# Performance work log

Hardware: AMD Instinct MI355X
Metric: run time of the kernel (lower is better)

## Reference

```python
import jax, jax.numpy as jnp
import numpy as np

D_IN, D, HEADS, DH, DEPTH, NMEM = 1024, 512, 4, 128, 2, 60


def _layernorm(x, g, b, eps=1e-5):
    m = x.mean(-1, keepdims=True)
    v = ((x - m) ** 2).mean(-1, keepdims=True)
    return (x - m) * jax.lax.rsqrt(v + eps) * g + b


def setup_inputs() -> dict:
    key = jax.random.key(0)
    ks = jax.random.split(key, 24)
    r = lambda i, shape, s=0.02: jax.random.normal(ks[i], shape, jnp.float32) * s
    inner = HEADS * DH  # 512
    inp = {
        "x": jax.random.normal(ks[0], (8, 2048, D_IN), jnp.float32),
        # Temporal conv1d (kernel=3, pad=1), WIO layout
        "conv_w": r(1, (3, D_IN, D)),
        "conv_b": jnp.zeros((D,), jnp.float32),
        # 2 transformer layers, stacked on leading axis
        "ln1_g": jnp.ones((DEPTH, D), jnp.float32),
        "ln1_b": jnp.zeros((DEPTH, D), jnp.float32),
        "qkv_w": r(2, (DEPTH, D, inner * 4)),
        "out_w": r(3, (DEPTH, 2 * inner, D)),
        "out_b": jnp.zeros((DEPTH, D), jnp.float32),
        "ln2_g": jnp.ones((DEPTH, D), jnp.float32),
        "ln2_b": jnp.zeros((DEPTH, D), jnp.float32),
        "ff_w1": r(4, (DEPTH, D, D)),
        "ff_b1": jnp.zeros((DEPTH, D), jnp.float32),
        "ff_w2": r(5, (DEPTH, D, D)),
        "ff_b2": jnp.zeros((DEPTH, D), jnp.float32),
        # memory banks (uniform +-1/sqrt(dim) per reset_parameters)
        "amem": jax.random.uniform(ks[6], (NMEM, D), jnp.float32, -1.0, 1.0) / np.sqrt(D),
        "nmem": jax.random.uniform(ks[7], (NMEM, D), jnp.float32, -1.0, 1.0) / np.sqrt(D),
        "enc_w": r(8, (D, D)),
        "enc_b": jnp.zeros((D,), jnp.float32),
        "cls_w1": r(9, (2 * D, 128)),
        "cls_b1": jnp.zeros((128,), jnp.float32),
        "cls_w2": r(10, (128, 1)),
        "cls_b2": jnp.zeros((1,), jnp.float32),
    }
    return inp


def _forward(x, conv_w, conv_b, ln1_g, ln1_b, qkv_w, out_w, out_b,
             ln2_g, ln2_b, ff_w1, ff_b1, ff_w2, ff_b2,
             amem, nmem, enc_w, enc_b, cls_w1, cls_b1, cls_w2, cls_b2):
    b, n, _ = x.shape
    # Temporal: conv1d k=3 same padding + ReLU -> (b, n, 512)
    h = jax.lax.conv_general_dilated(x, conv_w, (1,), "SAME",
                                     dimension_numbers=("NWC", "WIO", "NWC")) + conv_b
    h = jax.nn.relu(h)

    # fixed-decay attention matrix (same for all layers): exp(-|i-j|/e), col-sum normalized
    idx = jnp.arange(n, dtype=jnp.float32)
    A2 = jnp.exp(-jnp.abs(idx[:, None] - idx[None, :]) / jnp.e)  # (n, n)
    A2 = A2 / A2.sum(-1)  # torch broadcast: divide along last dim by row-sums (symmetric)

    scale = DH ** -0.5
    for l in range(DEPTH):
        xn = _layernorm(h, ln1_g[l], ln1_b[l])
        qkvt = xn @ qkv_w[l]  # (b, n, 4*inner)
        q, k, v, t = jnp.split(qkvt, 4, axis=-1)
        reshape = lambda a: a.reshape(b, n, HEADS, DH).transpose(0, 2, 1, 3)  # bhnd
        q, k, v, t = map(reshape, (q, k, v, t))
        attn1 = jax.nn.softmax(jnp.einsum("bhnd,bhmd->bhnm", q, k) * scale, axis=-1)
        o1 = jnp.einsum("bhnm,bhmd->bhnd", attn1, v)
        o2 = jnp.einsum("nm,bhmd->bhnd", A2, t)
        o = jnp.concatenate([o1, o2], axis=-1)  # (b, h, n, 2*dh)
        o = o.transpose(0, 2, 1, 3).reshape(b, n, 2 * HEADS * DH)
        h = o @ out_w[l] + out_b[l] + h
        xn2 = _layernorm(h, ln2_g[l], ln2_b[l])
        ff = jax.nn.gelu(xn2 @ ff_w1[l] + ff_b1[l], approximate=False) @ ff_w2[l] + ff_b2[l]
        h = ff + h

    # memory retrieval (augment path only; temporal_att discarded in Test forward)
    mscale = 1.0 / np.sqrt(D)
    a_att = jax.nn.sigmoid(jnp.einsum("btd,kd->btk", h, amem) * mscale)
    n_att = jax.nn.sigmoid(jnp.einsum("btd,kd->btk", h, nmem) * mscale)
    a_aug = jnp.einsum("btk,kd->btd", a_att, amem) @ enc_w + enc_b
    n_aug = jnp.einsum("btk,kd->btd", n_att, nmem) @ enc_w + enc_b

    z = jnp.concatenate([h, a_aug + n_aug], axis=-1)  # (b, n, 1024)
    pre = jax.nn.sigmoid(jax.nn.relu(z @ cls_w1 + cls_b1) @ cls_w2 + cls_b2)  # (b, n, 1)
    return pre.reshape(b, 1, -1).mean(1)  # (b, n)


def reference(x, conv_w, conv_b, ln1_g, ln1_b, qkv_w, out_w, out_b,
              ln2_g, ln2_b, ff_w1, ff_b1, ff_w2, ff_b2,
              amem, nmem, enc_w, enc_b, cls_w1, cls_b1, cls_w2, cls_b2):
    return _forward(x, conv_w, conv_b, ln1_g, ln1_b, qkv_w, out_w, out_b,
                    ln2_g, ln2_b, ff_w1, ff_b1, ff_w2, ff_b2,
                    amem, nmem, enc_w, enc_b, cls_w1, cls_b1, cls_w2, cls_b2)
```

## Files before the change

kernel.cpp:

```cpp
#include <hip/hip_runtime.h>
#include <hip/hip_bf16.h>
#include <math.h>

typedef __attribute__((ext_vector_type(4))) float f32x4;
typedef __attribute__((ext_vector_type(8))) short s16x8;
typedef unsigned short ushort_t;

__device__ __forceinline__ float bfbits2f(unsigned short u) {
  unsigned int x = ((unsigned int)u) << 16;
  return __builtin_bit_cast(float, x);
}
__device__ __forceinline__ unsigned short f2bfbits(float f) {
  unsigned int x = __builtin_bit_cast(unsigned int, f);
  unsigned int r = x + 0x7fffu + ((x >> 16) & 1u);
  return (unsigned short)(r >> 16);
}

__device__ __forceinline__ void gload_lds16(const ushort_t* g, ushort_t* l) {
  __builtin_amdgcn_global_load_lds(
      (const __attribute__((address_space(1))) unsigned int*)g,
      (__attribute__((address_space(3))) unsigned int*)l, 16, 0, 0);
}

#define ACT_NONE 0
#define ACT_RELU 1
#define ACT_GELU 2
#define ACT_SIGM 3

template<int ACT, bool OBF, bool BIAS, bool RES>
__global__ __launch_bounds__(256) void gemm_bf16(
    const ushort_t* __restrict__ A, const ushort_t* __restrict__ B,
    void* __restrict__ C, const float* __restrict__ bias, float bscale,
    const float* __restrict__ res,
    int K, int lda, int ldb, int ldc, float alpha, int nz2,
    long long sA1, long long sA2, long long sB1, long long sB2,
    long long sC1, long long sC2)
{
  const int z = blockIdx.z;
  const int z1 = z / nz2, z2 = z % nz2;
  const ushort_t* Ab = A + z1 * sA1 + z2 * sA2 + (long long)blockIdx.y * 128 * lda;
  const ushort_t* Bb = B + z1 * sB1 + z2 * sB2 + (long long)blockIdx.x * 128 * ldb;
  const long long coff = z1 * sC1 + z2 * sC2;

  __shared__ ushort_t As[128 * 64];
  __shared__ ushort_t Bs[128 * 64];

  const int tid = threadIdx.x;
  const int lane = tid & 63, wid = tid >> 6;
  const int wr = wid >> 1, wc = wid & 1;
  const int lr = lane & 15, lk = lane >> 4;

  f32x4 acc[4][4];
#pragma unroll
  for (int m = 0; m < 4; ++m)
#pragma unroll
    for (int n = 0; n < 4; ++n) {
      acc[m][n][0] = 0.f; acc[m][n][1] = 0.f; acc[m][n][2] = 0.f; acc[m][n][3] = 0.f;
    }

  const int nk = K >> 6;
  for (int kt = 0; kt < nk; ++kt) {
    const ushort_t* Ak = Ab + kt * 64;
    const ushort_t* Bk = Bb + kt * 64;
    __syncthreads();
#pragma unroll
    for (int i = 0; i < 4; ++i) {
      int c = wid * 4 + i;
      int row = c * 8 + (lane >> 3);
      int slot = (lane & 7) ^ (row & 7);
      gload_lds16(Ak + (long long)row * lda + slot * 8, As + c * 512);
      gload_lds16(Bk + (long long)row * ldb + slot * 8, Bs + c * 512);
    }
    __syncthreads();
#pragma unroll
    for (int kk = 0; kk < 2; ++kk) {
      s16x8 af[4], bv[4];
#pragma unroll
      for (int m = 0; m < 4; ++m) {
        int row = wr * 64 + m * 16 + lr;
        int cc = ((kk * 4 + lk) ^ (row & 7)) << 3;
        af[m] = *(const s16x8*)(&As[row * 64 + cc]);
      }
#pragma unroll
      for (int n = 0; n < 4; ++n) {
        int row = wc * 64 + n * 16 + lr;
        int cc = ((kk * 4 + lk) ^ (row & 7)) << 3;
        bv[n] = *(const s16x8*)(&Bs[row * 64 + cc]);
      }
#pragma unroll
      for (int m = 0; m < 4; ++m)
#pragma unroll
        for (int n = 0; n < 4; ++n)
          acc[m][n] = __builtin_amdgcn_mfma_f32_16x16x32_bf16(af[m], bv[n], acc[m][n], 0, 0, 0);
    }
  }

  const long long row0 = (long long)blockIdx.y * 128 + wr * 64 + lk * 4;
  const int col0 = blockIdx.x * 128 + wc * 64 + lr;
#pragma unroll
  for (int m = 0; m < 4; ++m)
#pragma unroll
    for (int n = 0; n < 4; ++n)
#pragma unroll
      for (int r = 0; r < 4; ++r) {
        long long row = row0 + m * 16 + r;
        int col = col0 + n * 16;
        float v = acc[m][n][r] * alpha;
        if (BIAS) v += bias[col] * bscale;
        if (RES) v += res[coff + row * ldc + col];
        if (ACT == ACT_RELU) v = fmaxf(v, 0.f);
        else if (ACT == ACT_GELU) v = 0.5f * v * (1.f + erff(v * 0.70710678118654752f));
        else if (ACT == ACT_SIGM) v = 1.f / (1.f + expf(-v));
        if (OBF) ((ushort_t*)C)[coff + row * ldc + col] = f2bfbits(v);
        else ((float*)C)[coff + row * ldc + col] = v;
      }
}

__global__ __launch_bounds__(256, 4) void flash_attn(
    const ushort_t* __restrict__ qkvt,
    const ushort_t* __restrict__ Vt,
    ushort_t* __restrict__ ob,
    float scale)
{
  const int qb = blockIdx.x;
  const int pair = blockIdx.y;
  const int b = pair >> 2, hh = pair & 3;

  const int tid = threadIdx.x;
  const int lane = tid & 63, w = tid >> 6;
  const int lr = lane & 15, lk = lane >> 4;

  __shared__ ushort_t Ks[64 * 128];
  __shared__ ushort_t Vs[128 * 64];
  __shared__ ushort_t Ps[4 * 16 * 64];

  const ushort_t* Qbase = qkvt + ((long long)(b * 2048 + qb * 64 + w * 16)) * 2048 + hh * 128;
  const ushort_t* Kbase = qkvt + ((long long)b * 2048) * 2048 + 512 + hh * 128;
  const ushort_t* Vbase = Vt + (long long)pair * 128 * 2048;
  ushort_t* Pw = &Ps[w * 16 * 64];

  s16x8 qf[4];
#pragma unroll
  for (int kf = 0; kf < 4; ++kf)
    qf[kf] = *(const s16x8*)(Qbase + (long long)lr * 2048 + kf * 32 + lk * 8);

  f32x4 accO[8];
#pragma unroll
  for (int n = 0; n < 8; ++n) { accO[n][0] = 0.f; accO[n][1] = 0.f; accO[n][2] = 0.f; accO[n][3] = 0.f; }
  float mrun[4], lpart[4];
#pragma unroll
  for (int r = 0; r < 4; ++r) { mrun[r] = -1e30f; lpart[r] = 0.f; }

  const float thr = 8.0f / scale;

  const int krow_l = lane >> 4;
  const int kslot_l = lane & 15;
  const int vrow_l = lane >> 3;
  const int vslot_l = lane & 7;

  for (int t = 0; t < 32; ++t) {
    __syncthreads();
#pragma unroll
    for (int i = 0; i < 4; ++i) {
      int c = w * 4 + i;
      int kr = c * 4 + krow_l;
      int ks_ = kslot_l ^ (kr & 7);
      gload_lds16(Kbase + (long long)(t * 64 + kr) * 2048 + ks_ * 8, Ks + c * 512);
      int vr = c * 8 + vrow_l;
      int vs_ = vslot_l ^ (vr & 7);
      gload_lds16(Vbase + (long long)vr * 2048 + t * 64 + vs_ * 8, Vs + c * 512);
    }
    __syncthreads();

    f32x4 accS[4];
#pragma unroll
    for (int n = 0; n < 4; ++n) { accS[n][0] = 0.f; accS[n][1] = 0.f; accS[n][2] = 0.f; accS[n][3] = 0.f; }
#pragma unroll
    for (int kf = 0; kf < 4; ++kf) {
#pragma unroll
      for (int n = 0; n < 4; ++n) {
        s16x8 kb = *(const s16x8*)(&Ks[(n * 16 + lr) * 128 + (((kf * 4 + lk) ^ (lr & 7)) << 3)]);
        accS[n] = __builtin_amdgcn_mfma_f32_16x16x32_bf16(qf[kf], kb, accS[n], 0, 0, 0);
      }
    }

    float vmx[4];
#pragma unroll
    for (int r = 0; r < 4; ++r)
      vmx[r] = fmaxf(fmaxf(accS[0][r], accS[1][r]), fmaxf(accS[2][r], accS[3][r]));
    bool ok = true;
#pragma unroll
    for (int r = 0; r < 4; ++r) ok &= (vmx[r] <= mrun[r] + thr);
    if (!__all(ok)) {
#pragma unroll
      for (int r = 0; r < 4; ++r) {
        float mx = vmx[r];
        mx = fmaxf(mx, __shfl_xor(mx, 1));
        mx = fmaxf(mx, __shfl_xor(mx, 2));
        mx = fmaxf(mx, __shfl_xor(mx, 4));
        mx = fmaxf(mx, __shfl_xor(mx, 8));
        float mn = fmaxf(mrun[r], mx);
        float al = __expf(scale * (mrun[r] - mn));
        mrun[r] = mn;
        lpart[r] *= al;
#pragma unroll
        for (int n = 0; n < 8; ++n) accO[n][r] *= al;
      }
    }
#pragma unroll
    for (int n = 0; n < 4; ++n)
#pragma unroll
      for (int r = 0; r < 4; ++r) {
        float pv = __expf(scale * (accS[n][r] - mrun[r]));
        lpart[r] += pv;
        int prow = lk * 4 + r;
        int gidx = (n * 2 + (lr >> 3)) ^ (prow & 7);
        Pw[prow * 64 + gidx * 8 + (lr & 7)] = f2bfbits(pv);
      }

#pragma unroll
    for (int ks = 0; ks < 2; ++ks) {
      s16x8 pa = *(const s16x8*)(&Pw[lr * 64 + (((ks * 4 + lk) ^ (lr & 7)) << 3)]);
#pragma unroll
      for (int n = 0; n < 8; ++n) {
        s16x8 vb = *(const s16x8*)(&Vs[(n * 16 + lr) * 64 + (((ks * 4 + lk) ^ (lr & 7)) << 3)]);
        accO[n] = __builtin_amdgcn_mfma_f32_16x16x32_bf16(pa, vb, accO[n], 0, 0, 0);
      }
    }
  }

#pragma unroll
  for (int r = 0; r < 4; ++r) {
    float s = lpart[r];
    s += __shfl_xor(s, 1);
    s += __shfl_xor(s, 2);
    s += __shfl_xor(s, 4);
    s += __shfl_xor(s, 8);
    float linv = 1.f / s;
    long long row = (long long)b * 2048 + qb * 64 + w * 16 + lk * 4 + r;
#pragma unroll
    for (int n = 0; n < 8; ++n)
      ob[row * 1024 + hh * 256 + n * 16 + lr] = f2bfbits(accO[n][r] * linv);
  }
}

__global__ __launch_bounds__(256) void ln_kernel(const float* __restrict__ h,
                                                 const float* __restrict__ g,
                                                 const float* __restrict__ b,
                                                 ushort_t* __restrict__ out)
{
  const int D = 512;
  long long row = blockIdx.x;
  const float* x = h + row * D;
  int t = threadIdx.x;
  float v0 = x[t], v1 = x[t + 256];
  __shared__ float rs[256], rss[256];
  rs[t] = v0 + v1; rss[t] = v0 * v0 + v1 * v1;
  __syncthreads();
  for (int o = 128; o > 0; o >>= 1) {
    if (t < o) { rs[t] += rs[t + o]; rss[t] += rss[t + o]; }
    __syncthreads();
  }
  float mean = rs[0] * (1.f / D);
  float var = rss[0] * (1.f / D) - mean * mean;
  float inv = rsqrtf(var + 1e-5f);
  out[row * D + t] = f2bfbits((v0 - mean) * inv * g[t] + b[t]);
  out[row * D + t + 256] = f2bfbits((v1 - mean) * inv * g[t + 256] + b[t + 256]);
}

__global__ __launch_bounds__(256) void build_xpad(const float* __restrict__ x,
                                                  ushort_t* __restrict__ xp)
{
  long long idx = (long long)blockIdx.x * 256 + threadIdx.x;
  int c = (int)(idx % 1024);
  long long t = idx / 1024;
  int r = (int)(t % 2050);
  int b = (int)(t / 2050);
  float v = (r == 0 || r == 2049) ? 0.f : x[((long long)b * 2048 + (r - 1)) * 1024 + c];
  xp[idx] = f2bfbits(v);
}

__global__ __launch_bounds__(256) void build_a2(ushort_t* __restrict__ A2)
{
  const int n = 2048;
  long long idx = (long long)blockIdx.x * 256 + threadIdx.x;
  int i = (int)(idx / n), j = (int)(idx % n);
  const float inv_e = 0.36787944117144233f;
  float w = expf(-fabsf((float)(i - j)) * inv_e);
  float r = expf(-inv_e);
  float geo = r / (1.f - r);
  float s = 1.f + geo * (1.f - expf(-inv_e * (float)j))
               + geo * (1.f - expf(-inv_e * (float)(n - 1 - j)));
  A2[idx] = f2bfbits(w / s);
}

__global__ __launch_bounds__(256) void tr_cast(const float* __restrict__ src0,
                                               ushort_t* __restrict__ dst0,
                                               int R, int C, long long ss, long long ds)
{
  const float* src = src0 + (long long)blockIdx.z * ss;
  ushort_t* dst = dst0 + (long long)blockIdx.z * ds;
  __shared__ float tile[32][33];
  int tx = threadIdx.x, ty = threadIdx.y;
#pragma unroll
  for (int i = 0; i < 4; ++i) {
    int r = blockIdx.y * 32 + ty + i * 8;
    int c = blockIdx.x * 32 + tx;
    tile[ty + i * 8][tx] = src[(long long)r * C + c];
  }
  __syncthreads();
#pragma unroll
  for (int i = 0; i < 4; ++i) {
    int rr = blockIdx.x * 32 + ty + i * 8;
    int cc = blockIdx.y * 32 + tx;
    dst[(long long)rr * R + cc] = f2bfbits(tile[tx][ty + i * 8]);
  }
}

__global__ __launch_bounds__(256) void tr_pair(const ushort_t* __restrict__ qkvt,
                                               ushort_t* __restrict__ out, int coloff)
{
  int p = blockIdx.z;
  int b = p >> 2, hh = p & 3;
  const ushort_t* src = qkvt + ((long long)b * 2048) * 2048 + coloff + hh * 128;
  ushort_t* dst = out + (long long)p * 128 * 2048;
  __shared__ ushort_t tile[32][33];
  int tx = threadIdx.x, ty = threadIdx.y;
  int n0 = blockIdx.x * 32, d0 = blockIdx.y * 32;
#pragma unroll
  for (int i = 0; i < 4; ++i)
    tile[ty + i * 8][tx] = src[(long long)(n0 + ty + i * 8) * 2048 + d0 + tx];
  __syncthreads();
#pragma unroll
  for (int i = 0; i < 4; ++i)
    dst[(long long)(d0 + ty + i * 8) * 2048 + n0 + tx] = tile[tx][ty + i * 8];
}

__global__ __launch_bounds__(256) void build_mem(const float* __restrict__ amem,
                                                 const float* __restrict__ nmem,
                                                 ushort_t* __restrict__ memc,
                                                 ushort_t* __restrict__ memTc)
{
  int idx = blockIdx.x * 256 + threadIdx.x;
  int r = idx / 512, d = idx % 512;
  float v = 0.f;
  if (r < 60) v = amem[r * 512 + d];
  else if (r >= 64 && r < 124) v = nmem[(r - 64) * 512 + d];
  unsigned short u = f2bfbits(v);
  memc[idx] = u;
  memTc[d * 128 + r] = u;
}

__global__ __launch_bounds__(256) void cast_rows(const float* __restrict__ src,
                                                 ushort_t* __restrict__ dst,
                                                 int cols, int ldd)
{
  long long idx = (long long)blockIdx.x * 256 + threadIdx.x;
  long long r = idx / cols;
  int c = (int)(idx % cols);
  dst[r * ldd + c] = f2bfbits(src[idx]);
}

__global__ __launch_bounds__(256) void cls2_kernel(const ushort_t* __restrict__ cls1,
                                                   const float* __restrict__ w2,
                                                   const float* __restrict__ b2,
                                                   float* __restrict__ out)
{
  int row = blockIdx.x * 4 + (threadIdx.x >> 6);
  int lane = threadIdx.x & 63;
  const ushort_t* rp = cls1 + (long long)row * 128;
  float v = bfbits2f(rp[lane]) * w2[lane] + bfbits2f(rp[lane + 64]) * w2[lane + 64];
#pragma unroll
  for (int m = 32; m > 0; m >>= 1) v += __shfl_xor(v, m, 64);
  if (lane == 0) out[row] = 1.f / (1.f + expf(-(v + b2[0])));
}

static inline void* carve(char*& p, size_t bytes) {
  void* r = (void*)p;
  p += (bytes + 255) & ~(size_t)255;
  return r;
}

template<int ACT, bool OBF, bool BIAS, bool RES>
static inline void gemm(hipStream_t st, const ushort_t* A, const ushort_t* B, void* C,
                        const float* bias, float bscale, const float* res,
                        int M, int N, int K, int lda, int ldb, int ldc, float alpha,
                        int Z, int nz2,
                        long long sA1, long long sA2, long long sB1, long long sB2,
                        long long sC1, long long sC2)
{
  dim3 grid(N / 128, M / 128, Z), blk(256, 1, 1);
  gemm_bf16<ACT, OBF, BIAS, RES><<<grid, blk, 0, st>>>(
      A, B, C, bias, bscale, res, K, lda, ldb, ldc, alpha, nz2,
      sA1, sA2, sB1, sB2, sC1, sC2);
}

extern "C" void kernel_launch(void* const* d_in, const int* in_sizes, int n_in,
                              void* d_out, int out_size, void* d_ws, size_t ws_size,
                              hipStream_t stream)
{
  (void)in_sizes; (void)n_in; (void)out_size; (void)ws_size;
  const float* x      = (const float*)d_in[0];
  const float* conv_w = (const float*)d_in[1];
  const float* conv_b = (const float*)d_in[2];
  const float* ln1_g  = (const float*)d_in[3];
  const float* ln1_b  = (const float*)d_in[4];
  const float* qkv_w  = (const float*)d_in[5];
  const float* out_w  = (const float*)d_in[6];
  const float* out_b  = (const float*)d_in[7];
  const float* ln2_g  = (const float*)d_in[8];
  const float* ln2_b  = (const float*)d_in[9];
  const float* ff_w1  = (const float*)d_in[10];
  const float* ff_b1  = (const float*)d_in[11];
  const float* ff_w2  = (const float*)d_in[12];
  const float* ff_b2  = (const float*)d_in[13];
  const float* amem   = (const float*)d_in[14];
  const float* nmem   = (const float*)d_in[15];
  const float* enc_w  = (const float*)d_in[16];
  const float* enc_b  = (const float*)d_in[17];
  const float* cls_w1 = (const float*)d_in[18];
  const float* cls_b1 = (const float*)d_in[19];
  const float* cls_w2 = (const float*)d_in[20];
  const float* cls_b2 = (const float*)d_in[21];
  float* outp = (float*)d_out;

  const long long M = 16384;
  const float att_scale = 0.08838834764831845f;
  const float mem_scale = 0.04419417382415922f;

  char* p = (char*)d_ws;
  float*    h    = (float*)   carve(p, (size_t)M * 512 * 4);
  ushort_t* A2b  = (ushort_t*)carve(p, (size_t)2048 * 2048 * 2);
  ushort_t* Wcat  = (ushort_t*)carve(p, (size_t)512 * 3072 * 2);
  ushort_t* qkvT  = (ushort_t*)carve(p, (size_t)2 * 2048 * 512 * 2);
  ushort_t* outT  = (ushort_t*)carve(p, (size_t)2 * 512 * 1024 * 2);
  ushort_t* f1T   = (ushort_t*)carve(p, (size_t)2 * 512 * 512 * 2);
  ushort_t* f2T   = (ushort_t*)carve(p, (size_t)2 * 512 * 512 * 2);
  ushort_t* encT  = (ushort_t*)carve(p, (size_t)512 * 512 * 2);
  ushort_t* c1T   = (ushort_t*)carve(p, (size_t)128 * 1024 * 2);
  ushort_t* memc  = (ushort_t*)carve(p, (size_t)128 * 512 * 2);
  ushort_t* memTc = (ushort_t*)carve(p, (size_t)512 * 128 * 2);
  char* U1 = (char*)carve(p, (size_t)8 * 2050 * 1024 * 2);
  ushort_t* xpad = (ushort_t*)U1;
  ushort_t* Vt   = (ushort_t*)U1;
  ushort_t* Tt   = (ushort_t*)(U1 + (size_t)32 * 128 * 2048 * 2);
  ushort_t* ffb  = (ushort_t*)U1;
  ushort_t* zb   = (ushort_t*)U1;
  char* U2 = (char*)carve(p, (size_t)M * 2048 * 2);
  ushort_t* qkvt  = (ushort_t*)U2;
  ushort_t* attb  = (ushort_t*)U2;
  ushort_t* m1b   = (ushort_t*)(U2 + (size_t)M * 128 * 2);
  ushort_t* cls1b = (ushort_t*)(U2 + (size_t)M * 128 * 2 + (size_t)M * 512 * 2);
  ushort_t* ob = (ushort_t*)carve(p, (size_t)M * 1024 * 2);
  ushort_t* xn = (ushort_t*)carve(p, (size_t)M * 512 * 2);

  dim3 tb(32, 8, 1);

  build_xpad<<<(8 * 2050 * 1024) / 256, 256, 0, stream>>>(x, xpad);
  build_a2<<<(2048 * 2048) / 256, 256, 0, stream>>>(A2b);
  tr_cast<<<dim3(512 / 32, 3072 / 32, 1), tb, 0, stream>>>(conv_w, Wcat, 3072, 512, 0, 0);
  tr_cast<<<dim3(2048 / 32, 512 / 32, 2), tb, 0, stream>>>(qkv_w, qkvT, 512, 2048,
      (long long)512 * 2048, (long long)2048 * 512);
  tr_cast<<<dim3(512 / 32, 1024 / 32, 2), tb, 0, stream>>>(out_w, outT, 1024, 512,
      (long long)1024 * 512, (long long)512 * 1024);
  tr_cast<<<dim3(512 / 32, 512 / 32, 2), tb, 0, stream>>>(ff_w1, f1T, 512, 512,
      (long long)512 * 512, (long long)512 * 512);
  tr_cast<<<dim3(512 / 32, 512 / 32, 2), tb, 0, stream>>>(ff_w2, f2T, 512, 512,
      (long long)512 * 512, (long long)512 * 512);
  tr_cast<<<dim3(512 / 32, 512 / 32, 1), tb, 0, stream>>>(enc_w, encT, 512, 512, 0, 0);
  tr_cast<<<dim3(128 / 32, 1024 / 32, 1), tb, 0, stream>>>(cls_w1, c1T, 1024, 128, 0, 0);
  build_mem<<<256, 256, 0, stream>>>(amem, nmem, memc, memTc);

  gemm<ACT_RELU, false, true, false>(stream, xpad, Wcat, h, conv_b, 1.f, nullptr,
      2048, 512, 3072, 1024, 3072, 512, 1.f,
      8, 8, 0, (long long)2050 * 1024, 0, 0, 0, (long long)2048 * 512);

  for (int l = 0; l < 2; ++l) {
    ln_kernel<<<16384, 256, 0, stream>>>(h, ln1_g + l * 512, ln1_b + l * 512, xn);
    gemm<ACT_NONE, true, false, false>(stream, xn, qkvT + (long long)l * 2048 * 512, qkvt,
        nullptr, 1.f, nullptr, 16384, 2048, 512, 512, 512, 2048, 1.f,
        1, 1, 0, 0, 0, 0, 0, 0);
    tr_pair<<<dim3(64, 4, 32), tb, 0, stream>>>(qkvt, Vt, 1024);
    tr_pair<<<dim3(64, 4, 32), tb, 0, stream>>>(qkvt, Tt, 1536);
    gemm<ACT_NONE, true, false, false>(stream, A2b, Tt, ob + 128, nullptr, 1.f, nullptr,
        2048, 128, 2048, 2048, 2048, 1024, 1.f,
        32, 4, 0, 0, (long long)4 * 128 * 2048, (long long)128 * 2048,
        (long long)2048 * 1024, 256);
    flash_attn<<<dim3(32, 32), 256, 0, stream>>>(qkvt, Vt, ob, att_scale);
    gemm<ACT_NONE, false, true, true>(stream, ob, outT + (long long)l * 512 * 1024, h,
        out_b + l * 512, 1.f, h, 16384, 512, 1024, 1024, 1024, 512, 1.f,
        1, 1, 0, 0, 0, 0, 0, 0);
    ln_kernel<<<16384, 256, 0, stream>>>(h, ln2_g + l * 512, ln2_b + l * 512, xn);
    gemm<ACT_GELU, true, true, false>(stream, xn, f1T + (long long)l * 512 * 512, ffb,
        ff_b1 + l * 512, 1.f, nullptr, 16384, 512, 512, 512, 512, 512, 1.f,
        1, 1, 0, 0, 0, 0, 0, 0);
    gemm<ACT_NONE, false, true, true>(stream, ffb, f2T + (long long)l * 512 * 512, h,
        ff_b2 + l * 512, 1.f, h, 16384, 512, 512, 512, 512, 512, 1.f,
        1, 1, 0, 0, 0, 0, 0, 0);
  }

  cast_rows<<<(16384 * 512) / 256, 256, 0, stream>>>(h, zb, 512, 1024);
  gemm<ACT_SIGM, true, false, false>(stream, zb, memc, attb, nullptr, 1.f, nullptr,
      16384, 128, 512, 1024, 512, 128, mem_scale, 1, 1, 0, 0, 0, 0, 0, 0);
  gemm<ACT_NONE, true, false, false>(stream, attb, memTc, m1b, nullptr, 1.f, nullptr,
      16384, 512, 128, 128, 128, 512, 1.f, 1, 1, 0, 0, 0, 0, 0, 0);
  gemm<ACT_NONE, true, true, false>(stream, m1b, encT, zb + 512, enc_b, 2.f, nullptr,
      16384, 512, 512, 512, 512, 1024, 1.f, 1, 1, 0, 0, 0, 0, 0, 0);
  gemm<ACT_RELU, true, true, false>(stream, zb, c1T, cls1b, cls_b1, 1.f, nullptr,
      16384, 128, 1024, 1024, 1024, 128, 1.f, 1, 1, 0, 0, 0, 0, 0, 0);
  cls2_kernel<<<4096, 256, 0, stream>>>(cls1b, cls_w2, cls_b2, outp);
}
```

Measured before the change: 995.8 us.

## Transpose QK^T MFMA to make softmax row-local and swizzle block order

```diff
diff --git a/kernel.cpp b/kernel.cpp
--- a/kernel.cpp
+++ b/kernel.cpp
@@ -4,6 +4,7 @@
 
 typedef __attribute__((ext_vector_type(4))) float f32x4;
 typedef __attribute__((ext_vector_type(8))) short s16x8;
+typedef __attribute__((ext_vector_type(2))) unsigned int u32x2;
 typedef unsigned short ushort_t;
 
 __device__ __forceinline__ float bfbits2f(unsigned short u) {
@@ -36,10 +37,17 @@
     long long sA1, long long sA2, long long sB1, long long sB2,
     long long sC1, long long sC2)
 {
-  const int z = blockIdx.z;
-  const int z1 = z / nz2, z2 = z % nz2;
-  const ushort_t* Ab = A + z1 * sA1 + z2 * sA2 + (long long)blockIdx.y * 128 * lda;
-  const ushort_t* Bb = B + z1 * sB1 + z2 * sB2 + (long long)blockIdx.x * 128 * ldb;
+  const int flat = blockIdx.x + gridDim.x * (blockIdx.y + gridDim.y * blockIdx.z);
+  const int cpx = (gridDim.x * gridDim.y * gridDim.z) >> 3;
+  const int sw = (flat & 7) * cpx + (flat >> 3);
+  const int bx = sw % gridDim.x;
+  const int rest = sw / gridDim.x;
+  const int by = rest % gridDim.y;
+  const int bz = rest / gridDim.y;
+
+  const int z1 = bz / nz2, z2 = bz % nz2;
+  const ushort_t* Ab = A + z1 * sA1 + z2 * sA2 + (long long)by * 128 * lda;
+  const ushort_t* Bb = B + z1 * sB1 + z2 * sB2 + (long long)bx * 128 * ldb;
   const long long coff = z1 * sC1 + z2 * sC2;
 
   __shared__ ushort_t As[128 * 64];
@@ -95,8 +103,8 @@
     }
   }
 
-  const long long row0 = (long long)blockIdx.y * 128 + wr * 64 + lk * 4;
-  const int col0 = blockIdx.x * 128 + wc * 64 + lr;
+  const long long row0 = (long long)by * 128 + wr * 64 + lk * 4;
+  const int col0 = bx * 128 + wc * 64 + lr;
 #pragma unroll
   for (int m = 0; m < 4; ++m)
 #pragma unroll
@@ -122,8 +130,11 @@
     ushort_t* __restrict__ ob,
     float scale)
 {
-  const int qb = blockIdx.x;
-  const int pair = blockIdx.y;
+  const int flat = blockIdx.x + gridDim.x * blockIdx.y;
+  const int cpx = (gridDim.x * gridDim.y) >> 3;
+  const int sw = (flat & 7) * cpx + (flat >> 3);
+  const int qb = sw % gridDim.x;
+  const int pair = sw / gridDim.x;
   const int b = pair >> 2, hh = pair & 3;
 
   const int tid = threadIdx.x;
@@ -147,10 +158,7 @@
   f32x4 accO[8];
 #pragma unroll
   for (int n = 0; n < 8; ++n) { accO[n][0] = 0.f; accO[n][1] = 0.f; accO[n][2] = 0.f; accO[n][3] = 0.f; }
-  float mrun[4], lpart[4];
-#pragma unroll
-  for (int r = 0; r < 4; ++r) { mrun[r] = -1e30f; lpart[r] = 0.f; }
-
+  float mrun = -1e30f, lpart = 0.f;
   const float thr = 8.0f / scale;
 
   const int krow_l = lane >> 4;
@@ -180,43 +188,48 @@
 #pragma unroll
       for (int n = 0; n < 4; ++n) {
         s16x8 kb = *(const s16x8*)(&Ks[(n * 16 + lr) * 128 + (((kf * 4 + lk) ^ (lr & 7)) << 3)]);
-        accS[n] = __builtin_amdgcn_mfma_f32_16x16x32_bf16(qf[kf], kb, accS[n], 0, 0, 0);
+        accS[n] = __builtin_amdgcn_mfma_f32_16x16x32_bf16(kb, qf[kf], accS[n], 0, 0, 0);
       }
     }
 
-    float vmx[4];
-#pragma unroll
-    for (int r = 0; r < 4; ++r)
-      vmx[r] = fmaxf(fmaxf(accS[0][r], accS[1][r]), fmaxf(accS[2][r], accS[3][r]));
-    bool ok = true;
-#pragma unroll
-    for (int r = 0; r < 4; ++r) ok &= (vmx[r] <= mrun[r] + thr);
-    if (!__all(ok)) {
-#pragma unroll
-      for (int r = 0; r < 4; ++r) {
-        float mx = vmx[r];
-        mx = fmaxf(mx, __shfl_xor(mx, 1));
-        mx = fmaxf(mx, __shfl_xor(mx, 2));
-        mx = fmaxf(mx, __shfl_xor(mx, 4));
-        mx = fmaxf(mx, __shfl_xor(mx, 8));
-        float mn = fmaxf(mrun[r], mx);
-        float al = __expf(scale * (mrun[r] - mn));
-        mrun[r] = mn;
-        lpart[r] *= al;
-#pragma unroll
-        for (int n = 0; n < 8; ++n) accO[n][r] *= al;
-      }
-    }
+    float vmx = accS[0][0];
 #pragma unroll
     for (int n = 0; n < 4; ++n)
 #pragma unroll
-      for (int r = 0; r < 4; ++r) {
-        float pv = __expf(scale * (accS[n][r] - mrun[r]));
-        lpart[r] += pv;
-        int prow = lk * 4 + r;
-        int gidx = (n * 2 + (lr >> 3)) ^ (prow & 7);
-        Pw[prow * 64 + gidx * 8 + (lr & 7)] = f2bfbits(pv);
-      }
+      for (int r = 0; r < 4; ++r) vmx = fmaxf(vmx, accS[n][r]);
+
+    if (!__all(vmx <= mrun + thr)) {
+      float mx = vmx;
+      mx = fmaxf(mx, __shfl_xor(mx, 16, 64));
+      mx = fmaxf(mx, __shfl_xor(mx, 32, 64));
+      float mn = fmaxf(mrun, mx);
+      float al = __expf(scale * (mrun - mn));
+      mrun = mn;
+      lpart *= al;
+      float alO[4];
+#pragma unroll
+      for (int r = 0; r < 4; ++r)
+        alO[r] = __shfl(al, (lane & 48) | (lk * 4 + r), 64);
+#pragma unroll
+      for (int n = 0; n < 8; ++n)
+#pragma unroll
+        for (int r = 0; r < 4; ++r) accO[n][r] *= alO[r];
+    }
+
+    const float sm = scale * mrun;
+#pragma unroll
+    for (int n = 0; n < 4; ++n) {
+      float p0 = __expf(scale * accS[n][0] - sm);
+      float p1 = __expf(scale * accS[n][1] - sm);
+      float p2 = __expf(scale * accS[n][2] - sm);
+      float p3 = __expf(scale * accS[n][3] - sm);
+      lpart += p0 + p1 + p2 + p3;
+      u32x2 pk;
+      pk[0] = (unsigned)f2bfbits(p0) | ((unsigned)f2bfbits(p1) << 16);
+      pk[1] = (unsigned)f2bfbits(p2) | ((unsigned)f2bfbits(p3) << 16);
+      int g = (n * 2 + (lk >> 1)) ^ (lr & 7);
+      *(u32x2*)(&Pw[lr * 64 + g * 8 + (lk & 1) * 4]) = pk;
+    }
 
 #pragma unroll
     for (int ks = 0; ks < 2; ++ks) {
@@ -229,18 +242,20 @@
     }
   }
 
+  float Lrow = lpart;
+  Lrow += __shfl_xor(Lrow, 16, 64);
+  Lrow += __shfl_xor(Lrow, 32, 64);
+  float linv_q = 1.f / Lrow;
+  float linvO[4];
+#pragma unroll
+  for (int r = 0; r < 4; ++r)
+    linvO[r] = __shfl(linv_q, (lane & 48) | (lk * 4 + r), 64);
 #pragma unroll
   for (int r = 0; r < 4; ++r) {
-    float s = lpart[r];
-    s += __shfl_xor(s, 1);
-    s += __shfl_xor(s, 2);
-    s += __shfl_xor(s, 4);
-    s += __shfl_xor(s, 8);
-    float linv = 1.f / s;
     long long row = (long long)b * 2048 + qb * 64 + w * 16 + lk * 4 + r;
 #pragma unroll
     for (int n = 0; n < 8; ++n)
-      ob[row * 1024 + hh * 256 + n * 16 + lr] = f2bfbits(accO[n][r] * linv);
+      ob[row * 1024 + hh * 256 + n * 16 + lr] = f2bfbits(accO[n][r] * linvO[r]);
   }
 }
 
```

New measurement: 937.4 us. -5.9%, faster.
